# Kernel tuning notes

Measured on AMD Instinct MI355X. Metric: run time of the kernel, lower is better.

## Reference

```python
import jax, jax.numpy as jnp
import numpy as np

BLOCK_SIZE = 64
IN_CHANNELS = 1024
OUT_CHANNELS = 1024
O_NBLOCKS = OUT_CHANNELS // BLOCK_SIZE  # 16
I_NBLOCKS = IN_CHANNELS // BLOCK_SIZE   # 16
N_TOKENS = 32768


def setup_inputs() -> dict:
    key = jax.random.key(0)
    kx, kw = jax.random.split(key)
    x = jax.random.normal(kx, (N_TOKENS, IN_CHANNELS), dtype=jnp.float32)
    # xavier_uniform over the (o_nblocks, i_nblocks, block_size) tensor:
    # fan_in = i_nblocks * block_size, fan_out = block_size (last-dim convention)
    fan_in = I_NBLOCKS * BLOCK_SIZE
    fan_out = BLOCK_SIZE
    limit = float(np.sqrt(6.0 / (fan_in + fan_out)))
    w = jax.random.uniform(kw, (O_NBLOCKS, I_NBLOCKS, BLOCK_SIZE),
                           dtype=jnp.float32, minval=-limit, maxval=limit)
    return {"x": x, "w": w}


def _build_dense_weight(w):
    # w: (R, Q, bs). Dense W[r*bs+i, q*bs+j] = w[r, q, (i - j) mod bs]
    R, Q, bs = w.shape
    i = jnp.arange(bs)
    idx = (i[:, None] - i[None, :]) % bs          # (bs, bs) circulant index
    Wb = w[:, :, idx]                              # (R, Q, bs, bs)
    return Wb.transpose(0, 2, 1, 3).reshape(R * bs, Q * bs)  # (out, in)


def reference(x, w):
    W = _build_dense_weight(w)                     # (out_channels, in_channels)
    return x @ W.T                                 # F.linear, no bias
```

## Files before the change

kernel.cpp:

```cpp
#include <hip/hip_runtime.h>
#include <stdint.h>


#define NTOK 32768
#define NCH  1024
#define NKT  16

typedef short bf16x8 __attribute__((ext_vector_type(8)));
typedef float f32x4  __attribute__((ext_vector_type(4)));
typedef unsigned short u16x8 __attribute__((ext_vector_type(8)));

static __device__ __forceinline__ unsigned short f2bf(float f) {
    unsigned int u = __float_as_uint(f);
    u += 0x7FFFu + ((u >> 16) & 1u);
    return (unsigned short)(u >> 16);
}

#define GLOAD16(gp, lp)                                                          \
    __builtin_amdgcn_global_load_lds(                                            \
        (const __attribute__((address_space(1))) unsigned int*)(gp),             \
        (__attribute__((address_space(3))) unsigned int*)(lp), 16, 0, 0)

__global__ void cvt_x_kernel(const float* __restrict__ x, unsigned short* __restrict__ xb) {
    int i = blockIdx.x * blockDim.x + threadIdx.x;
    int row = i >> 7;
    int j   = i & 127;
    const float4* src = (const float4*)(x + (((size_t)row) << 10) + (j << 3));
    float4 a = src[0], b = src[1];
    u16x8 v;
    v[0]=f2bf(a.x); v[1]=f2bf(a.y); v[2]=f2bf(a.z); v[3]=f2bf(a.w);
    v[4]=f2bf(b.x); v[5]=f2bf(b.y); v[6]=f2bf(b.z); v[7]=f2bf(b.w);
    int js = (j & ~7) | ((j & 7) ^ (row & 7));
    *(u16x8*)(xb + (((size_t)row) << 10) + (js << 3)) = v;
}

__global__ void build_w_kernel(const float* __restrict__ w, unsigned short* __restrict__ Wb) {
    int i = blockIdx.x * blockDim.x + threadIdx.x;
    int o = i >> 7;
    int j = i & 127;
    int r = o >> 6;
    int q = j >> 3;
    const float* wrow = w + ((r * 16 + q) << 6);
    int k0 = j << 3;
    u16x8 v;
#pragma unroll
    for (int e = 0; e < 8; ++e) v[e] = f2bf(wrow[(o - (k0 + e)) & 63]);
    int js = (j & ~7) | ((j & 7) ^ (o & 7));
    *(u16x8*)(Wb + (((size_t)o) << 10) + (js << 3)) = v;
}

#define BAR() __builtin_amdgcn_s_barrier()
#define LGKM0() asm volatile("s_waitcnt lgkmcnt(0)" ::: "memory")
#define VMCNT(n) asm volatile("s_waitcnt vmcnt(" #n ")" ::: "memory")
#define SETPRIO(n) __builtin_amdgcn_s_setprio(n)
#define MFMA4(d, av, bv) d = __builtin_amdgcn_mfma_f32_16x16x32_bf16(av, bv, d, 0, 0, 0)
#define NOHOOK ((void)0)

#define STAGE(bufA, bufB, t) do {                                                \
    const char* _sa = srcA + ((t) << 7);                                         \
    const char* _sb = srcB + ((t) << 7);                                         \
    char* _da = (bufA) + (wv << 10);                                             \
    char* _db = (bufB) + (wv << 10);                                             \
    GLOAD16(_sa, _da); GLOAD16(_sa + (64 << 11), _da + 8192);                    \
    GLOAD16(_sb, _db); GLOAD16(_sb + (64 << 11), _db + 8192);                    \
} while (0)

#define KSTEP2(Abuf, Bbuf, DO_STAGE, WN) do {                                    \
    bf16x8 afr[4][2], bfr[2][2];                                                 \
    _Pragma("unroll") for (int m = 0; m < 4; ++m)                                \
      _Pragma("unroll") for (int ks = 0; ks < 2; ++ks)                           \
        afr[m][ks] = *(const bf16x8*)((Abuf) + a_off[ks] + m * 2048);            \
    _Pragma("unroll") for (int n = 0; n < 2; ++n)                                \
      _Pragma("unroll") for (int ks = 0; ks < 2; ++ks)                           \
        bfr[n][ks] = *(const bf16x8*)((Bbuf) + b_off[ks] + n * 2048);            \
    LGKM0();                                                                     \
    BAR();                                                                       \
    DO_STAGE;                                                                    \
    SETPRIO(1);                                                                  \
    _Pragma("unroll") for (int m = 0; m < 4; ++m)                                \
      _Pragma("unroll") for (int n = 0; n < 2; ++n) {                            \
        MFMA4(acc[m][n], afr[m][0], bfr[n][0]);                                  \
        MFMA4(acc[m][n], afr[m][1], bfr[n][1]);                                  \
      }                                                                          \
    SETPRIO(0);                                                                  \
    WN;                                                                          \
    BAR();                                                                       \
} while (0)

__global__ void __launch_bounds__(512, 4) gemm128_kernel(const unsigned short* __restrict__ A,
                                                         const unsigned short* __restrict__ B,
                                                         float* __restrict__ C) {
    __shared__ __align__(16) char lds[65536];
    char* As0 = lds;
    char* As1 = lds + 16384;
    char* Bs0 = lds + 32768;
    char* Bs1 = lds + 49152;

    int tid  = threadIdx.x;
    int lane = tid & 63;
    int wv   = tid >> 6;
    int wr   = wv >> 2;
    int wc   = wv & 3;

    int cpx = gridDim.x >> 3;
    int wid = ((int)blockIdx.x & 7) * cpx + ((int)blockIdx.x >> 3);
    int tn = wid & 7, tm = wid >> 3;
    int m0 = tm * 128, n0 = tn * 128;

    const char* srcA = (const char*)A + (((size_t)(m0 + (tid >> 3))) << 11) + ((tid & 7) << 4);
    const char* srcB = (const char*)B + (((size_t)(n0 + (tid >> 3))) << 11) + ((tid & 7) << 4);

    int xa   = (lane & 7) << 4;
    int kq16 = (lane >> 4) << 4;
    int abase = (wr * 64 + (lane & 15)) * 128;
    int bbase = (wc * 32 + (lane & 15)) * 128;
    int a_off[2] = { abase + (kq16 ^ xa), abase + ((64 + kq16) ^ xa) };
    int b_off[2] = { bbase + (kq16 ^ xa), bbase + ((64 + kq16) ^ xa) };

    f32x4 acc[4][2] = {};

    STAGE(As0, Bs0, 0);
    STAGE(As1, Bs1, 1);
    VMCNT(4); BAR();

    for (int t = 0; t < 12; t += 2) {
        KSTEP2(As0, Bs0, STAGE(As0, Bs0, t + 2), VMCNT(4));
        KSTEP2(As1, Bs1, STAGE(As1, Bs1, t + 3), VMCNT(4));
    }
    KSTEP2(As0, Bs0, STAGE(As0, Bs0, 14), VMCNT(4));
    KSTEP2(As1, Bs1, STAGE(As1, Bs1, 15), VMCNT(4));
    KSTEP2(As0, Bs0, NOHOOK, VMCNT(0));
    {
        bf16x8 afr[4][2], bfr[2][2];
#pragma unroll
        for (int m = 0; m < 4; ++m)
#pragma unroll
            for (int ks = 0; ks < 2; ++ks)
                afr[m][ks] = *(const bf16x8*)(As1 + a_off[ks] + m * 2048);
#pragma unroll
        for (int n = 0; n < 2; ++n)
#pragma unroll
            for (int ks = 0; ks < 2; ++ks)
                bfr[n][ks] = *(const bf16x8*)(Bs1 + b_off[ks] + n * 2048);
        LGKM0();
        SETPRIO(1);
#pragma unroll
        for (int m = 0; m < 4; ++m)
#pragma unroll
            for (int n = 0; n < 2; ++n) {
                MFMA4(acc[m][n], afr[m][0], bfr[n][0]);
                MFMA4(acc[m][n], afr[m][1], bfr[n][1]);
            }
        SETPRIO(0);
    }

    float* Cp = C + ((size_t)(m0 + wr * 64)) * NCH + n0 + wc * 32;
    int cc = lane & 15;
    int rr = (lane >> 4) << 2;
#pragma unroll
    for (int m = 0; m < 4; ++m)
#pragma unroll
        for (int j = 0; j < 4; ++j) {
            float* rowp = Cp + ((size_t)(m * 16 + rr + j)) * NCH;
#pragma unroll
            for (int n = 0; n < 2; ++n)
                rowp[n * 16 + cc] = acc[m][n][j];
        }
}

__global__ void naive_kernel(const float* __restrict__ x, const float* __restrict__ w,
                             float* __restrict__ out) {
    int t = blockIdx.x;
    int o = blockIdx.y * 256 + threadIdx.x;
    const float* xr = x + (size_t)t * NCH;
    int r = o >> 6, oi = o & 63;
    float s = 0.f;
    for (int q = 0; q < 16; ++q) {
        const float* wq = w + (r * 16 + q) * 64;
        const float* xq = xr + q * 64;
#pragma unroll 8
        for (int j = 0; j < 64; ++j) s += xq[j] * wq[(oi - j) & 63];
    }
    out[(size_t)t * NCH + o] = s;
}

extern "C" void kernel_launch(void* const* d_in, const int* in_sizes, int n_in,
                              void* d_out, int out_size, void* d_ws, size_t ws_size,
                              hipStream_t stream) {
    const float* x = (const float*)d_in[0];
    const float* w = (const float*)d_in[1];
    float* out = (float*)d_out;

    const size_t needX = (size_t)NTOK * NCH * sizeof(unsigned short);
    const size_t needW = (size_t)NCH * NCH * sizeof(unsigned short);

    if (ws_size >= needX + needW) {
        unsigned short* xb = (unsigned short*)d_ws;
        unsigned short* Wb = (unsigned short*)((char*)d_ws + needX);
        hipLaunchKernelGGL(cvt_x_kernel, dim3(NTOK * 128 / 256), dim3(256), 0, stream, x, xb);
        hipLaunchKernelGGL(build_w_kernel, dim3(NCH * 128 / 256), dim3(256), 0, stream, w, Wb);
        hipLaunchKernelGGL(gemm128_kernel, dim3(2048), dim3(512), 0, stream, xb, Wb, out);
    } else {
        hipLaunchKernelGGL(naive_kernel, dim3(NTOK, 4), dim3(256), 0, stream, x, w, out);
    }
}
```

Before: 109.5 us.

## Fuse fp32-to-bf16 conversion of x into GEMM tile loads

Drops the separate cvt_x pass. The GEMM now streams fp32 x tiles straight into LDS with a swizzled layout and converts them to bf16 in registers (v_cvt_pk_bf16_f32) right before the MFMAs. This removes a full write and re-read of a 64 MB bf16 copy of x. In exchange the A tile doubles in LDS (96 KB total), launch bounds drop to 1 block per CU, and every A fragment costs extra LDS reads and convert instructions.

```diff
diff --git a/kernel.cpp b/kernel.cpp
--- a/kernel.cpp
+++ b/kernel.cpp
@@ -21,17 +21,13 @@
         (const __attribute__((address_space(1))) unsigned int*)(gp),             \
         (__attribute__((address_space(3))) unsigned int*)(lp), 16, 0, 0)
 
-__global__ void cvt_x_kernel(const float* __restrict__ x, unsigned short* __restrict__ xb) {
-    int i = blockIdx.x * blockDim.x + threadIdx.x;
-    int row = i >> 7;
-    int j   = i & 127;
-    const float4* src = (const float4*)(x + (((size_t)row) << 10) + (j << 3));
-    float4 a = src[0], b = src[1];
-    u16x8 v;
-    v[0]=f2bf(a.x); v[1]=f2bf(a.y); v[2]=f2bf(a.z); v[3]=f2bf(a.w);
-    v[4]=f2bf(b.x); v[5]=f2bf(b.y); v[6]=f2bf(b.z); v[7]=f2bf(b.w);
-    int js = (j & ~7) | ((j & 7) ^ (row & 7));
-    *(u16x8*)(xb + (((size_t)row) << 10) + (js << 3)) = v;
+static __device__ __forceinline__ bf16x8 cvt8(f32x4 l, f32x4 h) {
+    union { unsigned int w[4]; bf16x8 v; } u;
+    asm("v_cvt_pk_bf16_f32 %0, %1, %2" : "=v"(u.w[0]) : "v"(l[0]), "v"(l[1]));
+    asm("v_cvt_pk_bf16_f32 %0, %1, %2" : "=v"(u.w[1]) : "v"(l[2]), "v"(l[3]));
+    asm("v_cvt_pk_bf16_f32 %0, %1, %2" : "=v"(u.w[2]) : "v"(h[0]), "v"(h[1]));
+    asm("v_cvt_pk_bf16_f32 %0, %1, %2" : "=v"(u.w[3]) : "v"(h[2]), "v"(h[3]));
+    return u.v;
 }
 
 __global__ void build_w_kernel(const float* __restrict__ w, unsigned short* __restrict__ Wb) {
@@ -56,20 +52,30 @@
 #define MFMA4(d, av, bv) d = __builtin_amdgcn_mfma_f32_16x16x32_bf16(av, bv, d, 0, 0, 0)
 #define NOHOOK ((void)0)
 
-#define STAGE(bufA, bufB, t) do {                                                \
-    const char* _sa = srcA + ((t) << 7);                                         \
-    const char* _sb = srcB + ((t) << 7);                                         \
-    char* _da = (bufA) + (wv << 10);                                             \
-    char* _db = (bufB) + (wv << 10);                                             \
-    GLOAD16(_sa, _da); GLOAD16(_sa + (64 << 11), _da + 8192);                    \
-    GLOAD16(_sb, _db); GLOAD16(_sb + (64 << 11), _db + 8192);                    \
+#define STAGE_A(buf, t) do {                                                     \
+    const char* _s = srcA + ((t) << 8);                                          \
+    char* _d = (buf) + (wv << 10);                                               \
+    GLOAD16(_s,                        _d);                                      \
+    GLOAD16(_s + ((size_t)64 << 12),   _d + 8192);                               \
+    GLOAD16(_s + 128,                  _d + 16384);                              \
+    GLOAD16(_s + 128 + ((size_t)64 << 12), _d + 24576);                          \
+} while (0)
+
+#define STAGE_B(buf, t) do {                                                     \
+    const char* _s = srcB + ((t) << 7);                                          \
+    char* _d = (buf) + (wv << 10);                                               \
+    GLOAD16(_s, _d);                                                             \
+    GLOAD16(_s + ((size_t)64 << 11), _d + 8192);                                 \
 } while (0)
 
 #define KSTEP2(Abuf, Bbuf, DO_STAGE, WN) do {                                    \
     bf16x8 afr[4][2], bfr[2][2];                                                 \
     _Pragma("unroll") for (int m = 0; m < 4; ++m)                                \
-      _Pragma("unroll") for (int ks = 0; ks < 2; ++ks)                           \
-        afr[m][ks] = *(const bf16x8*)((Abuf) + a_off[ks] + m * 2048);            \
+      _Pragma("unroll") for (int ks = 0; ks < 2; ++ks) {                         \
+        f32x4 _lo = *(const f32x4*)((Abuf) + a_rd[ks][0] + m * 2048);            \
+        f32x4 _hi = *(const f32x4*)((Abuf) + a_rd[ks][1] + m * 2048);            \
+        afr[m][ks] = cvt8(_lo, _hi);                                             \
+      }                                                                          \
     _Pragma("unroll") for (int n = 0; n < 2; ++n)                                \
       _Pragma("unroll") for (int ks = 0; ks < 2; ++ks)                           \
         bfr[n][ks] = *(const bf16x8*)((Bbuf) + b_off[ks] + n * 2048);            \
@@ -87,14 +93,14 @@
     BAR();                                                                       \
 } while (0)
 
-__global__ void __launch_bounds__(512, 4) gemm128_kernel(const unsigned short* __restrict__ A,
-                                                         const unsigned short* __restrict__ B,
-                                                         float* __restrict__ C) {
-    __shared__ __align__(16) char lds[65536];
+__global__ void __launch_bounds__(512, 1) gemm_fused_kernel(const float* __restrict__ X,
+                                                            const unsigned short* __restrict__ B,
+                                                            float* __restrict__ C) {
+    __shared__ __align__(16) char lds[98304];
     char* As0 = lds;
-    char* As1 = lds + 16384;
-    char* Bs0 = lds + 32768;
-    char* Bs1 = lds + 49152;
+    char* As1 = lds + 32768;
+    char* Bs0 = lds + 65536;
+    char* Bs1 = lds + 81920;
 
     int tid  = threadIdx.x;
     int lane = tid & 63;
@@ -107,36 +113,51 @@
     int tn = wid & 7, tm = wid >> 3;
     int m0 = tm * 128, n0 = tn * 128;
 
-    const char* srcA = (const char*)A + (((size_t)(m0 + (tid >> 3))) << 11) + ((tid & 7) << 4);
+    int row0 = tid >> 3;
+    int gx   = (tid & 7) ^ (row0 & 7);
+    int lg   = ((gx & 3) << 1) | (gx >> 2);
+    const char* srcA = (const char*)X + (((size_t)(m0 + row0)) << 12) + (lg << 4);
+
     const char* srcB = (const char*)B + (((size_t)(n0 + (tid >> 3))) << 11) + ((tid & 7) << 4);
 
-    int xa   = (lane & 7) << 4;
-    int kq16 = (lane >> 4) << 4;
+    int p = lane & 7;
+    int q = lane >> 4;
     int abase = (wr * 64 + (lane & 15)) * 128;
+    int a_rd[2][2];
+#pragma unroll
+    for (int ks = 0; ks < 2; ++ks)
+#pragma unroll
+        for (int h = 0; h < 2; ++h)
+            a_rd[ks][h] = ks * 16384 + abase + (((q | (h << 2)) ^ p) << 4);
+
+    int kq16 = q << 4;
     int bbase = (wc * 32 + (lane & 15)) * 128;
-    int a_off[2] = { abase + (kq16 ^ xa), abase + ((64 + kq16) ^ xa) };
-    int b_off[2] = { bbase + (kq16 ^ xa), bbase + ((64 + kq16) ^ xa) };
+    int b_off[2] = { bbase + ((kq16 + 0)  ^ (p << 4)),
+                     bbase + ((kq16 + 64) ^ (p << 4)) };
 
     f32x4 acc[4][2] = {};
 
-    STAGE(As0, Bs0, 0);
-    STAGE(As1, Bs1, 1);
-    VMCNT(4); BAR();
+    STAGE_A(As0, 0); STAGE_B(Bs0, 0);
+    STAGE_A(As1, 1); STAGE_B(Bs1, 1);
+    VMCNT(6); BAR();
 
     for (int t = 0; t < 12; t += 2) {
-        KSTEP2(As0, Bs0, STAGE(As0, Bs0, t + 2), VMCNT(4));
-        KSTEP2(As1, Bs1, STAGE(As1, Bs1, t + 3), VMCNT(4));
-    }
-    KSTEP2(As0, Bs0, STAGE(As0, Bs0, 14), VMCNT(4));
-    KSTEP2(As1, Bs1, STAGE(As1, Bs1, 15), VMCNT(4));
+        KSTEP2(As0, Bs0, { STAGE_A(As0, t + 2); STAGE_B(Bs0, t + 2); }, VMCNT(6));
+        KSTEP2(As1, Bs1, { STAGE_A(As1, t + 3); STAGE_B(Bs1, t + 3); }, VMCNT(6));
+    }
+    KSTEP2(As0, Bs0, { STAGE_A(As0, 14); STAGE_B(Bs0, 14); }, VMCNT(6));
+    KSTEP2(As1, Bs1, { STAGE_A(As1, 15); STAGE_B(Bs1, 15); }, VMCNT(6));
     KSTEP2(As0, Bs0, NOHOOK, VMCNT(0));
     {
         bf16x8 afr[4][2], bfr[2][2];
 #pragma unroll
         for (int m = 0; m < 4; ++m)
 #pragma unroll
-            for (int ks = 0; ks < 2; ++ks)
-                afr[m][ks] = *(const bf16x8*)(As1 + a_off[ks] + m * 2048);
+            for (int ks = 0; ks < 2; ++ks) {
+                f32x4 _lo = *(const f32x4*)(As1 + a_rd[ks][0] + m * 2048);
+                f32x4 _hi = *(const f32x4*)(As1 + a_rd[ks][1] + m * 2048);
+                afr[m][ks] = cvt8(_lo, _hi);
+            }
 #pragma unroll
         for (int n = 0; n < 2; ++n)
 #pragma unroll
@@ -175,9 +196,9 @@
     const float* xr = x + (size_t)t * NCH;
     int r = o >> 6, oi = o & 63;
     float s = 0.f;
-    for (int q = 0; q < 16; ++q) {
-        const float* wq = w + (r * 16 + q) * 64;
-        const float* xq = xr + q * 64;
+    for (int qq = 0; qq < 16; ++qq) {
+        const float* wq = w + (r * 16 + qq) * 64;
+        const float* xq = xr + qq * 64;
 #pragma unroll 8
         for (int j = 0; j < 64; ++j) s += xq[j] * wq[(oi - j) & 63];
     }
@@ -191,15 +212,12 @@
     const float* w = (const float*)d_in[1];
     float* out = (float*)d_out;
 
-    const size_t needX = (size_t)NTOK * NCH * sizeof(unsigned short);
     const size_t needW = (size_t)NCH * NCH * sizeof(unsigned short);
 
-    if (ws_size >= needX + needW) {
-        unsigned short* xb = (unsigned short*)d_ws;
-        unsigned short* Wb = (unsigned short*)((char*)d_ws + needX);
-        hipLaunchKernelGGL(cvt_x_kernel, dim3(NTOK * 128 / 256), dim3(256), 0, stream, x, xb);
+    if (ws_size >= needW) {
+        unsigned short* Wb = (unsigned short*)d_ws;
         hipLaunchKernelGGL(build_w_kernel, dim3(NCH * 128 / 256), dim3(256), 0, stream, w, Wb);
-        hipLaunchKernelGGL(gemm128_kernel, dim3(2048), dim3(512), 0, stream, xb, Wb, out);
+        hipLaunchKernelGGL(gemm_fused_kernel, dim3(2048), dim3(512), 0, stream, x, Wb, out);
     } else {
         hipLaunchKernelGGL(naive_kernel, dim3(NTOK, 4), dim3(256), 0, stream, x, w, out);
     }
```

Result: slower. 135.6 us (+23.8%).
